# Kernel optimization log

Measured on AMD Instinct MI355X. Metric: run time of the kernel, lower is better.

The kernel has to match this reference:

```python
import jax, jax.numpy as jnp
import numpy as np

SEQ, IN_DIM, HID_DIM, OUT_DIM, WIDTH, DEPTH = 8192, 1024, 1024, 1024, 2048, 3


def setup_inputs() -> dict:
    key = jax.random.key(0)
    ks = jax.random.split(key, 8)
    s = lambda fi, fo: 1.0 / np.sqrt(fi)  # torch Linear default init scale
    return {
        "x": jax.random.normal(ks[0], (SEQ, IN_DIM), dtype=jnp.float32),
        "W0": jax.random.uniform(ks[1], (IN_DIM + HID_DIM, WIDTH), jnp.float32, -s(IN_DIM + HID_DIM, WIDTH), s(IN_DIM + HID_DIM, WIDTH)),
        "b0": jax.random.uniform(ks[2], (WIDTH,), jnp.float32, -s(IN_DIM + HID_DIM, WIDTH), s(IN_DIM + HID_DIM, WIDTH)),
        "Wmid": jax.random.uniform(ks[3], (DEPTH, WIDTH, WIDTH), jnp.float32, -s(WIDTH, WIDTH), s(WIDTH, WIDTH)),
        "bmid": jax.random.uniform(ks[4], (DEPTH, WIDTH), jnp.float32, -s(WIDTH, WIDTH), s(WIDTH, WIDTH)),
        "Wf": jax.random.uniform(ks[5], (WIDTH, HID_DIM + OUT_DIM), jnp.float32, -s(WIDTH, HID_DIM + OUT_DIM), s(WIDTH, HID_DIM + OUT_DIM)),
        "bf": jax.random.uniform(ks[6], (HID_DIM + OUT_DIM,), jnp.float32, -s(WIDTH, HID_DIM + OUT_DIM), s(WIDTH, HID_DIM + OUT_DIM)),
    }


def _mlp(f, W0, b0, Wmid, bmid, Wf, bf):
    # f: [in_dim + hid_dim]
    h = f @ W0 + b0
    for i in range(DEPTH):  # fixed small depth
        h = jax.nn.relu(h) @ Wmid[i] + bmid[i]
    return jax.nn.relu(h) @ Wf + bf  # [hid_dim + out_dim]


def reference(x, W0, b0, Wmid, bmid, Wf, bf):
    def step(hidden, x_t):
        feat = jnp.concatenate([x_t, hidden], axis=-1)
        o = _mlp(feat, W0, b0, Wmid, bmid, Wf, bf)
        return o[:HID_DIM], o[HID_DIM:]

    hidden0 = jnp.zeros((HID_DIM,), dtype=x.dtype)
    hidden, outputs = jax.lax.scan(step, hidden0, x)
    # match torch: hidden returned with leading singleton batch dim
    return hidden[None, :], outputs
```

## Files before the change

kernel.cpp:

```cpp
#include <hip/hip_runtime.h>
#include <hip/hip_bf16.h>
#include <stdint.h>

#define SEQ     8192
#define DIM     2048
#define HID     1024
#define NWG     256
#define CPW     8

typedef unsigned long long u64;
typedef __attribute__((ext_vector_type(4))) unsigned int u32x4;


__device__ __forceinline__ uint16_t f2bf(float f) {
  union { float f; uint32_t u; } v; v.f = f;
  uint32_t r = v.u + 0x7FFFu + ((v.u >> 16) & 1u);
  return (uint16_t)(r >> 16);
}
__device__ __forceinline__ float bf2f(uint16_t u) {
  union { uint32_t u; float f; } v; v.u = ((uint32_t)u) << 16; return v.f;
}
__device__ __forceinline__ void cstore64(u64* p, u64 v) {
  __hip_atomic_store(p, v, __ATOMIC_RELAXED, __HIP_MEMORY_SCOPE_AGENT);
}
__device__ __forceinline__ u64 pack2(float v0, float v1, uint32_t tag) {
  const uint32_t w0 = (uint32_t)f2bf(v0) | (tag << 16);
  const uint32_t w1 = (uint32_t)f2bf(v1) | (tag << 16);
  return ((u64)w1 << 32) | (u64)w0;
}
__device__ __forceinline__ u32x4 cload128(const void* p) {
  u32x4 r;
  asm volatile("global_load_dwordx4 %0, %1, off sc0 sc1"
               : "=v"(r) : "v"(p) : "memory");
  return r;
}
__device__ __forceinline__ void vm_drain() {
  asm volatile("s_waitcnt vmcnt(0)" ::: "memory");
  __builtin_amdgcn_sched_barrier(0);
}

__device__ __forceinline__ void poll_stage(const uint32_t* __restrict__ buf,
                                           int chunk, uint32_t thr,
                                           float* __restrict__ d) {
  const uint32_t* p = buf + (size_t)chunk * 16;
  u32x4 a, b;
  for (;;) {
    a = cload128(p);
    b = cload128(p + 4);
    vm_drain();
    bool ok = true;
    #pragma unroll
    for (int i = 0; i < 4; ++i) {
      ok &= (a[i] >= thr);
      ok &= (b[i] >= thr);
    }
    if (__all(ok)) break;
    __builtin_amdgcn_s_sleep(1);
  }
  #pragma unroll
  for (int i = 0; i < 4; ++i) {
    d[i]     = fmaxf(__uint_as_float(a[i] << 16), 0.f);
    d[4 + i] = fmaxf(__uint_as_float(b[i] << 16), 0.f);
  }
}

__global__ void k_hb(const float* __restrict__ W0, const float* __restrict__ b0,
                     const float* __restrict__ bfv, float* __restrict__ hb) {
  const int j = blockIdx.x * 256 + threadIdx.x;
  float acc = b0[j];
  for (int m = 0; m < HID; ++m)
    acc = fmaf(bfv[m], W0[(size_t)(HID + m) * DIM + j], acc);
  hb[j] = acc;
}

__global__ void k_G(const float* __restrict__ W0, const float* __restrict__ Wf,
                    float* __restrict__ Gt) {
  const int j = blockIdx.x * 16 + threadIdx.x;
  const int k = blockIdx.y * 16 + threadIdx.y;
  float acc = 0.f;
  for (int m = 0; m < HID; ++m)
    acc = fmaf(Wf[(size_t)k * DIM + m], W0[(size_t)(HID + m) * DIM + j], acc);
  Gt[(size_t)j * DIM + k] = acc;
}

__global__ void k_XC(const float* __restrict__ x, const float* __restrict__ W0,
                     const float* __restrict__ b0, const float* __restrict__ hb,
                     float* __restrict__ out, uint16_t* __restrict__ xct) {
  const int j = blockIdx.x * 16 + threadIdx.x;
  const int t = blockIdx.y * 16 + threadIdx.y;
  float acc = 0.f;
  for (int m = 0; m < HID; ++m)
    acc = fmaf(x[(size_t)t * HID + m], W0[(size_t)m * DIM + j], acc);
  acc += (t > 0) ? hb[j] : b0[j];
  const uint16_t v = f2bf(acc);
  if (t <= SEQ - 3) ((uint16_t*)(out + HID + (size_t)(t + 2) * HID))[j] = v;
  else              xct[(size_t)(t - (SEQ - 2)) * DIM + j] = v;
}

__global__ void __launch_bounds__(256, 1)
rnn_persist(const float* __restrict__ Wmid, const float* __restrict__ bmid,
            const float* __restrict__ Wf, const float* __restrict__ bfv,
            float* __restrict__ out, uint32_t* __restrict__ a0b,
            uint32_t* __restrict__ a1b, uint32_t* __restrict__ a2b,
            uint32_t* __restrict__ a3b, const float* __restrict__ Gt,
            const uint16_t* __restrict__ xct)
{
  __shared__ uint16_t wlds[3 * CPW * DIM];
  __shared__ uint16_t wflds[4 * DIM];
  __shared__ float    sAct[2][DIM];
  __shared__ u64      sG[2][4];

  const int tid  = threadIdx.x;
  const int wg   = blockIdx.x;
  const int wave = tid >> 6;
  const int lane = tid & 63;

  const int cidx0 = wave * 2;
  const int col0  = wg * CPW + cidx0;
  const int col1  = col0 + 1;
  const int ocol  = wg * 4 + wave;

  for (int i = tid; i < 3 * CPW * DIM; i += 256) {
    const int l = i >> 14;
    const int r = i & 16383;
    const int k = r >> 3;
    const int c = r & 7;
    wlds[(l * CPW + c) * DIM + k] =
        f2bf(Wmid[(size_t)l * DIM * DIM + (size_t)k * DIM + (wg * CPW + c)]);
  }
  for (int i = tid; i < 4 * DIM; i += 256) {
    const int w = i >> 11;
    const int k = i & 2047;
    wflds[w * DIM + k] = f2bf(Wf[(size_t)k * DIM + HID + wg * 4 + w]);
  }
  float4 gf0[8], gf1[8];
  #pragma unroll
  for (int j = 0; j < 8; ++j) {
    const int k = j * 256 + lane * 4;
    gf0[j] = *(const float4*)(Gt + (size_t)col0 * DIM + k);
    gf1[j] = *(const float4*)(Gt + (size_t)col1 * DIM + k);
  }
  if (tid < 8) sG[tid >> 2][tid & 3] = 0;
  __syncthreads();

  float bm0[3], bm1[3];
  #pragma unroll
  for (int l = 0; l < 3; ++l) {
    bm0[l] = bmid[l * DIM + col0];
    bm1[l] = bmid[l * DIM + col1];
  }
  const float bo = bfv[HID + ocol];

  uint32_t ph = 0;

  for (int t = 0; t < SEQ; ++t) {
    {
      const int par = (int)(ph & 1u);
      float* __restrict__ sa = sAct[par];
      const uint16_t* xcrow = (t <= SEQ - 3)
          ? (const uint16_t*)(out + HID + (size_t)(t + 2) * HID)
          : (xct + (size_t)(t - (SEQ - 2)) * DIM);
      const uint32_t xcw = *(const uint32_t*)(xcrow + col0);

      poll_stage(a3b, wave * 64 + lane, (4u * (uint32_t)t) << 16,
                 sa + wave * 512 + lane * 8);
      __syncthreads();

      float acc0 = 0.f, acc1 = 0.f, accO = 0.f;
      #pragma unroll
      for (int j = 0; j < 8; ++j) {
        const int kb = j * 256 + lane * 4;
        const float4 a = *(const float4*)&sa[kb];
        const float4 g0 = gf0[j], g1 = gf1[j];
        const ushort4 wo = *(const ushort4*)(wflds + wave * DIM + kb);
        acc0 = fmaf(a.x, g0.x, acc0); acc1 = fmaf(a.x, g1.x, acc1);
        acc0 = fmaf(a.y, g0.y, acc0); acc1 = fmaf(a.y, g1.y, acc1);
        acc0 = fmaf(a.z, g0.z, acc0); acc1 = fmaf(a.z, g1.z, acc1);
        acc0 = fmaf(a.w, g0.w, acc0); acc1 = fmaf(a.w, g1.w, acc1);
        accO = fmaf(a.x, bf2f(wo.x), accO);
        accO = fmaf(a.y, bf2f(wo.y), accO);
        accO = fmaf(a.z, bf2f(wo.z), accO);
        accO = fmaf(a.w, bf2f(wo.w), accO);
      }
      #pragma unroll
      for (int off = 32; off > 0; off >>= 1) {
        acc0 += __shfl_xor(acc0, off, 64);
        acc1 += __shfl_xor(acc1, off, 64);
        accO += __shfl_xor(accO, off, 64);
      }
      const uint32_t tag = 4u * (uint32_t)t + 1u;
      if (lane == 0) {
        const float v0 = acc0 + bf2f((uint16_t)(xcw & 0xFFFFu));
        const float v1 = acc1 + bf2f((uint16_t)(xcw >> 16));
        __hip_atomic_store(&sG[par][wave], pack2(v0, v1, tag),
                           __ATOMIC_RELAXED, __HIP_MEMORY_SCOPE_WORKGROUP);
        if (t > 0)
          out[HID + (size_t)(t - 1) * HID + ocol] = accO + bo;
      }
      if (wave == 0 && lane < 4) {
        const uint32_t thr = tag << 16;
        u64 pv;
        for (;;) {
          pv = __hip_atomic_load(&sG[par][lane], __ATOMIC_RELAXED,
                                 __HIP_MEMORY_SCOPE_WORKGROUP);
          if ((uint32_t)pv >= thr && (uint32_t)(pv >> 32) >= thr) break;
        }
        cstore64((u64*)a0b + wg * 8 + lane, pv);
      }
      ++ph;
    }
    #pragma unroll
    for (int l = 1; l < 4; ++l) {
      const int par = (int)(ph & 1u);
      float* __restrict__ sa = sAct[par];
      const uint32_t* src = (l == 1) ? a0b : ((l == 2) ? a1b : a2b);
      uint32_t* dst = (l == 1) ? a1b : ((l == 2) ? a2b : a3b);
      poll_stage(src, wave * 64 + lane,
                 (4u * (uint32_t)t + (uint32_t)l) << 16,
                 sa + wave * 512 + lane * 8);
      __syncthreads();

      float acc0 = 0.f, acc1 = 0.f;
      const uint16_t* w0p = wlds + (((l - 1) * CPW + cidx0) * DIM);
      const uint16_t* w1p = w0p + DIM;
      #pragma unroll
      for (int j = 0; j < 8; ++j) {
        const int kb = j * 256 + lane * 4;
        const float4  a  = *(const float4*)&sa[kb];
        const ushort4 wa = *(const ushort4*)(w0p + kb);
        const ushort4 wb = *(const ushort4*)(w1p + kb);
        acc0 = fmaf(a.x, bf2f(wa.x), acc0); acc1 = fmaf(a.x, bf2f(wb.x), acc1);
        acc0 = fmaf(a.y, bf2f(wa.y), acc0); acc1 = fmaf(a.y, bf2f(wb.y), acc1);
        acc0 = fmaf(a.z, bf2f(wa.z), acc0); acc1 = fmaf(a.z, bf2f(wb.z), acc1);
        acc0 = fmaf(a.w, bf2f(wa.w), acc0); acc1 = fmaf(a.w, bf2f(wb.w), acc1);
      }
      #pragma unroll
      for (int off = 32; off > 0; off >>= 1) {
        acc0 += __shfl_xor(acc0, off, 64);
        acc1 += __shfl_xor(acc1, off, 64);
      }
      const uint32_t tag = 4u * (uint32_t)t + (uint32_t)l + 1u;
      if (lane == 0) {
        __hip_atomic_store(&sG[par][wave],
                           pack2(acc0 + bm0[l - 1], acc1 + bm1[l - 1], tag),
                           __ATOMIC_RELAXED, __HIP_MEMORY_SCOPE_WORKGROUP);
      }
      if (wave == 0 && lane < 4) {
        const uint32_t thr = tag << 16;
        u64 pv;
        for (;;) {
          pv = __hip_atomic_load(&sG[par][lane], __ATOMIC_RELAXED,
                                 __HIP_MEMORY_SCOPE_WORKGROUP);
          if ((uint32_t)pv >= thr && (uint32_t)(pv >> 32) >= thr) break;
        }
        cstore64((u64*)dst + wg * 8 + lane, pv);
      }
      ++ph;
    }
  }

  {
    float* __restrict__ sa = sAct[ph & 1u];
    poll_stage(a3b, wave * 64 + lane, (4u * (uint32_t)SEQ) << 16,
               sa + wave * 512 + lane * 8);
    __syncthreads();
    float accO = 0.f, accH = 0.f;
    #pragma unroll
    for (int j = 0; j < 8; ++j) {
      const int kb = j * 256 + lane * 4;
      const float4  a  = *(const float4*)&sa[kb];
      const ushort4 wo = *(const ushort4*)(wflds + wave * DIM + kb);
      accO = fmaf(a.x, bf2f(wo.x), accO);
      accO = fmaf(a.y, bf2f(wo.y), accO);
      accO = fmaf(a.z, bf2f(wo.z), accO);
      accO = fmaf(a.w, bf2f(wo.w), accO);
      accH = fmaf(a.x, Wf[(size_t)(kb + 0) * DIM + ocol], accH);
      accH = fmaf(a.y, Wf[(size_t)(kb + 1) * DIM + ocol], accH);
      accH = fmaf(a.z, Wf[(size_t)(kb + 2) * DIM + ocol], accH);
      accH = fmaf(a.w, Wf[(size_t)(kb + 3) * DIM + ocol], accH);
    }
    #pragma unroll
    for (int off = 32; off > 0; off >>= 1) {
      accO += __shfl_xor(accO, off, 64);
      accH += __shfl_xor(accH, off, 64);
    }
    if (lane == 0) {
      out[HID + (size_t)(SEQ - 1) * HID + ocol] = accO + bo;
      out[ocol] = accH + bfv[ocol];
    }
  }
}

extern "C" void kernel_launch(void* const* d_in, const int* in_sizes, int n_in,
                              void* d_out, int out_size, void* d_ws, size_t ws_size,
                              hipStream_t stream) {
  (void)in_sizes; (void)n_in; (void)out_size; (void)ws_size;
  const float* x    = (const float*)d_in[0];
  const float* W0   = (const float*)d_in[1];
  const float* b0   = (const float*)d_in[2];
  const float* Wmid = (const float*)d_in[3];
  const float* bmid = (const float*)d_in[4];
  const float* Wf   = (const float*)d_in[5];
  const float* bfv  = (const float*)d_in[6];
  float* out = (float*)d_out;

  uint8_t* ws = (uint8_t*)d_ws;
  uint32_t* a0b = (uint32_t*)(ws + 0);
  uint32_t* a1b = (uint32_t*)(ws + 16384);
  uint32_t* a2b = (uint32_t*)(ws + 32768);
  uint32_t* a3b = (uint32_t*)(ws + 49152);
  uint16_t* xct = (uint16_t*)(ws + 65536);
  float*    hb  = (float*)(ws + 73728);
  float*    Gt  = (float*)(ws + 81920);

  hipMemsetAsync(d_ws, 0, 65536, stream);

  k_hb<<<dim3(8), dim3(256), 0, stream>>>(W0, b0, bfv, hb);
  k_G<<<dim3(128, 128), dim3(16, 16), 0, stream>>>(W0, Wf, Gt);
  k_XC<<<dim3(128, 512), dim3(16, 16), 0, stream>>>(x, W0, b0, hb, out, xct);

  rnn_persist<<<dim3(NWG), dim3(256), 0, stream>>>(
      Wmid, bmid, Wf, bfv, out, a0b, a1b, a2b, a3b, Gt, xct);
}
```

Measured before the change: 111.5 ms.

## Replace per-stage workgroup barrier with per-wave LDS flags and rotated chunk order

Each wave publishes an LDS flag once its slice of the activation vector is in shared memory, instead of every wave waiting at __syncthreads. Each wave first consumes its own slice, then the other waves' slices in rotated order, spinning on their flags only when it reaches them. The G-matrix register preload is reordered to match the rotated order. This aims to overlap the arrival skew between waves with useful compute, at the cost of LDS spin loops and relaxed-ordering correctness risk.

```diff
diff --git a/kernel.cpp b/kernel.cpp
--- a/kernel.cpp
+++ b/kernel.cpp
@@ -62,6 +62,13 @@
     d[i]     = fmaxf(__uint_as_float(a[i] << 16), 0.f);
     d[4 + i] = fmaxf(__uint_as_float(b[i] << 16), 0.f);
   }
+}
+
+__device__ __forceinline__ void lds_spin(uint32_t* f, uint32_t want) {
+  while (__hip_atomic_load(f, __ATOMIC_RELAXED,
+                           __HIP_MEMORY_SCOPE_WORKGROUP) < want) {}
+  asm volatile("" ::: "memory");
+  __builtin_amdgcn_sched_barrier(0);
 }
 
 __global__ void k_hb(const float* __restrict__ W0, const float* __restrict__ b0,
@@ -109,6 +116,7 @@
   __shared__ uint16_t wflds[4 * DIM];
   __shared__ float    sAct[2][DIM];
   __shared__ u64      sG[2][4];
+  __shared__ uint32_t sflag[2][4];
 
   const int tid  = threadIdx.x;
   const int wg   = blockIdx.x;
@@ -135,12 +143,19 @@
   }
   float4 gf0[8], gf1[8];
   #pragma unroll
-  for (int j = 0; j < 8; ++j) {
-    const int k = j * 256 + lane * 4;
-    gf0[j] = *(const float4*)(Gt + (size_t)col0 * DIM + k);
-    gf1[j] = *(const float4*)(Gt + (size_t)col1 * DIM + k);
-  }
-  if (tid < 8) sG[tid >> 2][tid & 3] = 0;
+  for (int qi = 0; qi < 4; ++qi) {
+    const int q = (wave + qi) & 3;
+    #pragma unroll
+    for (int jj = 0; jj < 2; ++jj) {
+      const int k = (2 * q + jj) * 256 + lane * 4;
+      gf0[qi * 2 + jj] = *(const float4*)(Gt + (size_t)col0 * DIM + k);
+      gf1[qi * 2 + jj] = *(const float4*)(Gt + (size_t)col1 * DIM + k);
+    }
+  }
+  if (tid < 8) {
+    sG[tid >> 2][tid & 3] = 0;
+    sflag[tid >> 2][tid & 3] = 0;
+  }
   __syncthreads();
 
   float bm0[3], bm1[3];
@@ -157,6 +172,7 @@
     {
       const int par = (int)(ph & 1u);
       float* __restrict__ sa = sAct[par];
+      const uint32_t want = ph + 1u;
       const uint16_t* xcrow = (t <= SEQ - 3)
           ? (const uint16_t*)(out + HID + (size_t)(t + 2) * HID)
           : (xct + (size_t)(t - (SEQ - 2)) * DIM);
@@ -164,23 +180,32 @@
 
       poll_stage(a3b, wave * 64 + lane, (4u * (uint32_t)t) << 16,
                  sa + wave * 512 + lane * 8);
-      __syncthreads();
+      asm volatile("s_waitcnt lgkmcnt(0)" ::: "memory");
+      __builtin_amdgcn_sched_barrier(0);
+      if (lane == 0)
+        __hip_atomic_store(&sflag[par][wave], want, __ATOMIC_RELAXED,
+                           __HIP_MEMORY_SCOPE_WORKGROUP);
 
       float acc0 = 0.f, acc1 = 0.f, accO = 0.f;
       #pragma unroll
-      for (int j = 0; j < 8; ++j) {
-        const int kb = j * 256 + lane * 4;
-        const float4 a = *(const float4*)&sa[kb];
-        const float4 g0 = gf0[j], g1 = gf1[j];
-        const ushort4 wo = *(const ushort4*)(wflds + wave * DIM + kb);
-        acc0 = fmaf(a.x, g0.x, acc0); acc1 = fmaf(a.x, g1.x, acc1);
-        acc0 = fmaf(a.y, g0.y, acc0); acc1 = fmaf(a.y, g1.y, acc1);
-        acc0 = fmaf(a.z, g0.z, acc0); acc1 = fmaf(a.z, g1.z, acc1);
-        acc0 = fmaf(a.w, g0.w, acc0); acc1 = fmaf(a.w, g1.w, acc1);
-        accO = fmaf(a.x, bf2f(wo.x), accO);
-        accO = fmaf(a.y, bf2f(wo.y), accO);
-        accO = fmaf(a.z, bf2f(wo.z), accO);
-        accO = fmaf(a.w, bf2f(wo.w), accO);
+      for (int qi = 0; qi < 4; ++qi) {
+        const int q = (wave + qi) & 3;
+        if (qi > 0) lds_spin(&sflag[par][q], want);
+        #pragma unroll
+        for (int jj = 0; jj < 2; ++jj) {
+          const int kb = (2 * q + jj) * 256 + lane * 4;
+          const float4 a = *(const float4*)&sa[kb];
+          const float4 g0 = gf0[qi * 2 + jj], g1 = gf1[qi * 2 + jj];
+          const ushort4 wo = *(const ushort4*)(wflds + wave * DIM + kb);
+          acc0 = fmaf(a.x, g0.x, acc0); acc1 = fmaf(a.x, g1.x, acc1);
+          acc0 = fmaf(a.y, g0.y, acc0); acc1 = fmaf(a.y, g1.y, acc1);
+          acc0 = fmaf(a.z, g0.z, acc0); acc1 = fmaf(a.z, g1.z, acc1);
+          acc0 = fmaf(a.w, g0.w, acc0); acc1 = fmaf(a.w, g1.w, acc1);
+          accO = fmaf(a.x, bf2f(wo.x), accO);
+          accO = fmaf(a.y, bf2f(wo.y), accO);
+          accO = fmaf(a.z, bf2f(wo.z), accO);
+          accO = fmaf(a.w, bf2f(wo.w), accO);
+        }
       }
       #pragma unroll
       for (int off = 32; off > 0; off >>= 1) {
@@ -213,26 +238,36 @@
     for (int l = 1; l < 4; ++l) {
       const int par = (int)(ph & 1u);
       float* __restrict__ sa = sAct[par];
+      const uint32_t want = ph + 1u;
       const uint32_t* src = (l == 1) ? a0b : ((l == 2) ? a1b : a2b);
       uint32_t* dst = (l == 1) ? a1b : ((l == 2) ? a2b : a3b);
       poll_stage(src, wave * 64 + lane,
                  (4u * (uint32_t)t + (uint32_t)l) << 16,
                  sa + wave * 512 + lane * 8);
-      __syncthreads();
+      asm volatile("s_waitcnt lgkmcnt(0)" ::: "memory");
+      __builtin_amdgcn_sched_barrier(0);
+      if (lane == 0)
+        __hip_atomic_store(&sflag[par][wave], want, __ATOMIC_RELAXED,
+                           __HIP_MEMORY_SCOPE_WORKGROUP);
 
       float acc0 = 0.f, acc1 = 0.f;
       const uint16_t* w0p = wlds + (((l - 1) * CPW + cidx0) * DIM);
       const uint16_t* w1p = w0p + DIM;
       #pragma unroll
-      for (int j = 0; j < 8; ++j) {
-        const int kb = j * 256 + lane * 4;
-        const float4  a  = *(const float4*)&sa[kb];
-        const ushort4 wa = *(const ushort4*)(w0p + kb);
-        const ushort4 wb = *(const ushort4*)(w1p + kb);
-        acc0 = fmaf(a.x, bf2f(wa.x), acc0); acc1 = fmaf(a.x, bf2f(wb.x), acc1);
-        acc0 = fmaf(a.y, bf2f(wa.y), acc0); acc1 = fmaf(a.y, bf2f(wb.y), acc1);
-        acc0 = fmaf(a.z, bf2f(wa.z), acc0); acc1 = fmaf(a.z, bf2f(wb.z), acc1);
-        acc0 = fmaf(a.w, bf2f(wa.w), acc0); acc1 = fmaf(a.w, bf2f(wb.w), acc1);
+      for (int qi = 0; qi < 4; ++qi) {
+        const int q = (wave + qi) & 3;
+        if (qi > 0) lds_spin(&sflag[par][q], want);
+        #pragma unroll
+        for (int jj = 0; jj < 2; ++jj) {
+          const int kb = (2 * q + jj) * 256 + lane * 4;
+          const float4  a  = *(const float4*)&sa[kb];
+          const ushort4 wa = *(const ushort4*)(w0p + kb);
+          const ushort4 wb = *(const ushort4*)(w1p + kb);
+          acc0 = fmaf(a.x, bf2f(wa.x), acc0); acc1 = fmaf(a.x, bf2f(wb.x), acc1);
+          acc0 = fmaf(a.y, bf2f(wa.y), acc0); acc1 = fmaf(a.y, bf2f(wb.y), acc1);
+          acc0 = fmaf(a.z, bf2f(wa.z), acc0); acc1 = fmaf(a.z, bf2f(wb.z), acc1);
+          acc0 = fmaf(a.w, bf2f(wa.w), acc0); acc1 = fmaf(a.w, bf2f(wb.w), acc1);
+        }
       }
       #pragma unroll
       for (int off = 32; off > 0; off >>= 1) {
```

New measurement: 108.7 ms, median of 2. 2.5% less time.
